# Optimization experiments

Measured on AMD Instinct MI355X. Metric: run time of the kernel, lower is better.

Reference implementation:

```python
import jax, jax.numpy as jnp
import numpy as np

B, C_IN, C_INTER, H, W_DIM = 8, 512, 256, 64, 64


def setup_inputs() -> dict:
    key = jax.random.key(0)
    k1, k2, k3, k4 = jax.random.split(key, 4)
    x = jax.random.normal(k1, (B, C_IN, H, W_DIM), dtype=jnp.float32)
    pem_feats = jax.random.normal(k2, (B, C_INTER, H * W_DIM), dtype=jnp.float32)
    # 1x1 conv weight stored as [out, in] (kernel spatial dims are 1x1)
    W = jax.random.normal(k3, (C_INTER, C_IN), dtype=jnp.float32) * (1.0 / np.sqrt(C_IN))
    bias = jax.random.normal(k4, (C_INTER,), dtype=jnp.float32) * 0.01
    return {"x": x, "pem_feats": pem_feats, "W": W, "bias": bias}


def reference(x, pem_feats, W, bias):
    b, c, h, w = x.shape
    # 1x1 conv == channel-mixing GEMM: [b, inter, h, w]
    proj = jnp.einsum('bchw,oc->bohw', x, W) + bias[None, :, None, None]
    proj = proj.reshape(b, -1, h * w)                      # [b, inter, hw]
    # weights[b,i,j] = <proj[:, i], pem[:, j]>  -> [b, hw, hw], softmax over j
    scores = jnp.einsum('bci,bcj->bij', proj, pem_feats)
    weights = jax.nn.softmax(scores, axis=-1)
    # out[b,k,i] = sum_j weights[b,j,i] * pem[b,k,j]
    eam = jnp.einsum('bji,bkj->bki', weights, pem_feats)   # [b, inter, hw]
    return eam.reshape(b, -1, h, w)
```

## Files before the change

kernel.cpp:

```cpp
#include <hip/hip_runtime.h>
#include <math.h>

#define BATCH 8
#define CIN 512
#define CO 256
#define HW 4096
#define KT 32
#define NSEG 4
#define SEGC 32

typedef unsigned short ushort_t;
typedef unsigned int uint_t;
typedef _Float16 v8h __attribute__((ext_vector_type(8)));
typedef _Float16 v4h __attribute__((ext_vector_type(4)));
typedef float v4f __attribute__((ext_vector_type(4)));
typedef ushort_t u16x8 __attribute__((ext_vector_type(8)));

__device__ __forceinline__ ushort_t f2h(float f) {
  return __builtin_bit_cast(ushort_t, (_Float16)f);
}
__device__ __forceinline__ v4f mfma16h(v8h a, v8h b, v4f c) {
  return __builtin_amdgcn_mfma_f32_16x16x32_f16(a, b, c, 0, 0, 0);
}
__device__ __forceinline__ v8h lds_frag_h512(const unsigned char* base, int row, int cb) {
  uint4 v = *(const uint4*)(base + row * 512 + (((cb) ^ (row & 7)) << 4));
  return __builtin_bit_cast(v8h, v);
}
__device__ __forceinline__ v8h lds_frag_h128(const unsigned char* base, int row, int cb) {
  uint4 v = *(const uint4*)(base + row * 128 + (((cb) ^ (row & 7)) << 4));
  return __builtin_bit_cast(v8h, v);
}
__device__ __forceinline__ void gll16(const void* g, void* l) {
  __builtin_amdgcn_global_load_lds(
      (const __attribute__((address_space(1))) unsigned int*)g,
      (__attribute__((address_space(3))) unsigned int*)l, 16, 0, 0);
}

__global__ __launch_bounds__(256) void k_w(
    const float* __restrict__ W, ushort_t* __restrict__ w_h) {
  int idx = blockIdx.x * 256 + threadIdx.x;
  size_t off = (size_t)idx * 8;
  float4 v0 = *(const float4*)&W[off];
  float4 v1 = *(const float4*)&W[off + 4];
  float f[8] = {v0.x, v0.y, v0.z, v0.w, v1.x, v1.y, v1.z, v1.w};
  u16x8 h;
#pragma unroll
  for (int j = 0; j < 8; ++j) h[j] = f2h(f[j]);
  *(u16x8*)&w_h[off] = h;
}

__global__ __launch_bounds__(256) void k_tr_x(
    const float* __restrict__ x, ushort_t* __restrict__ xt_h) {
  __shared__ float T[64][65];
  const int i0 = blockIdx.x * 64;
  const int c0 = blockIdx.y * 64;
  const int b  = blockIdx.z;
  const int t  = threadIdx.x;
  const int cl = t >> 4;
  const int i4 = (t & 15) * 4;
#pragma unroll
  for (int r = 0; r < 4; ++r) {
    int c = c0 + r * 16 + cl;
    size_t off = ((size_t)b * CIN + c) * HW + i0 + i4;
    float4 v = *(const float4*)&x[off];
    T[r * 16 + cl][i4 + 0] = v.x;
    T[r * 16 + cl][i4 + 1] = v.y;
    T[r * 16 + cl][i4 + 2] = v.z;
    T[r * 16 + cl][i4 + 3] = v.w;
  }
  __syncthreads();
  {
    int il = t >> 2;
    int cs = (t & 3) * 16;
    u16x8 h0, h1;
#pragma unroll
    for (int j = 0; j < 8; ++j) h0[j] = f2h(T[cs + j][il]);
#pragma unroll
    for (int j = 0; j < 8; ++j) h1[j] = f2h(T[cs + 8 + j][il]);
    size_t ro = ((size_t)b * HW + i0 + il) * CIN + c0 + cs;
    *(u16x8*)&xt_h[ro]     = h0;
    *(u16x8*)&xt_h[ro + 8] = h1;
  }
}

__global__ __launch_bounds__(256, 2) void k_proj_mfma(
    const ushort_t* __restrict__ xt_h, const ushort_t* __restrict__ w_h,
    const float* __restrict__ bias, ushort_t* __restrict__ proj_h) {
  __shared__ __align__(16) unsigned char L[2][128 * 128];
  const int bid = blockIdx.x;
  const int b = bid & 7;
  const int rest = bid >> 3;
  const int xt = rest & 31;
  const int oh = rest >> 5;
  const int x0 = xt * 128;
  const int t = threadIdx.x;
  const int lane = t & 63, wave = t >> 6;

  v4f acc[2][8];
#pragma unroll
  for (int xf = 0; xf < 2; ++xf)
#pragma unroll
    for (int of = 0; of < 8; ++of) acc[xf][of] = (v4f){0.f, 0.f, 0.f, 0.f};

  float bias_of[8];
#pragma unroll
  for (int of = 0; of < 8; ++of)
    bias_of[of] = bias[oh * 128 + of * 16 + (lane & 15)];

  for (int ch = 0; ch < 8; ++ch) {
    const int c0 = ch * 64;
#pragma unroll
    for (int i = 0; i < 4; ++i) {
      int G = i * 256 + t;
      int r = G >> 3, sl = G & 7;
      int cg = (sl ^ (r & 7)) << 3;
      size_t xsrc = ((size_t)b * HW + x0 + r) * CIN + c0 + cg;
      size_t wsrc = ((size_t)(oh * 128 + r)) * CIN + c0 + cg;
      unsigned lb = (unsigned)((i * 256 + wave * 64) << 4);
      gll16(&xt_h[xsrc], &L[0][lb]);
      gll16(&w_h[wsrc],  &L[1][lb]);
    }
    __syncthreads();
#pragma unroll
    for (int st = 0; st < 2; ++st) {
      int cb = st * 4 + (lane >> 4);
      v8h ah0 = lds_frag_h128(L[0], wave * 32 + (lane & 15), cb);
      v8h ah1 = lds_frag_h128(L[0], wave * 32 + 16 + (lane & 15), cb);
#pragma unroll
      for (int of = 0; of < 8; ++of) {
        v8h bh = lds_frag_h128(L[1], of * 16 + (lane & 15), cb);
        acc[0][of] = mfma16h(ah0, bh, acc[0][of]);
        acc[1][of] = mfma16h(ah1, bh, acc[1][of]);
      }
    }
    __syncthreads();
  }

  ushort_t* Th = (ushort_t*)&L[0][0];
#pragma unroll
  for (int xf = 0; xf < 2; ++xf)
#pragma unroll
    for (int of = 0; of < 8; ++of)
#pragma unroll
      for (int r = 0; r < 4; ++r) {
        int x_loc = wave * 32 + xf * 16 + (lane >> 4) * 4 + r;
        int o_loc = of * 16 + (lane & 15);
        Th[x_loc * 128 + o_loc] = f2h(acc[xf][of][r] + bias_of[of]);
      }
  __syncthreads();
  {
    int row = t >> 1, half = t & 1;
    size_t off = ((size_t)b * HW + x0 + row) * CO + oh * 128 + half * 64;
#pragma unroll
    for (int j = 0; j < 8; ++j)
      *(uint4*)&proj_h[off + j * 8] =
          *(const uint4*)&Th[row * 128 + half * 64 + j * 8];
  }
}

__global__ __launch_bounds__(256) void k_tr_pem(
    const float* __restrict__ pem,
    ushort_t* __restrict__ pem_t_h, ushort_t* __restrict__ pem_h) {
  __shared__ float T[64][65];
  const int y0 = blockIdx.x * 64;
  const int c0 = blockIdx.y * 64;
  const int b  = blockIdx.z;
  const int t  = threadIdx.x;
  const int cl = t >> 4;
  const int y4 = (t & 15) * 4;
#pragma unroll
  for (int r = 0; r < 4; ++r) {
    int c = c0 + r * 16 + cl;
    size_t off = ((size_t)b * CO + c) * HW + y0 + y4;
    float4 v = *(const float4*)&pem[off];
    ushort4 h;
    h.x = f2h(v.x); h.y = f2h(v.y); h.z = f2h(v.z); h.w = f2h(v.w);
    *(ushort4*)&pem_h[off] = h;
    T[r * 16 + cl][y4 + 0] = v.x;
    T[r * 16 + cl][y4 + 1] = v.y;
    T[r * 16 + cl][y4 + 2] = v.z;
    T[r * 16 + cl][y4 + 3] = v.w;
  }
  __syncthreads();
  {
    int yl = t >> 2;
    int cs = (t & 3) * 16;
    u16x8 h0, h1;
#pragma unroll
    for (int j = 0; j < 8; ++j) h0[j] = f2h(T[cs + j][yl]);
#pragma unroll
    for (int j = 0; j < 8; ++j) h1[j] = f2h(T[cs + 8 + j][yl]);
    size_t ro = ((size_t)b * HW + y0 + yl) * CO + c0 + cs;
    *(u16x8*)&pem_t_h[ro]     = h0;
    *(u16x8*)&pem_t_h[ro + 8] = h1;
  }
}

__global__ __launch_bounds__(512, 2) void k_stats_f16(
    const ushort_t* __restrict__ proj_h, const ushort_t* __restrict__ pem_t_h,
    float* __restrict__ m_seg, float* __restrict__ d_seg) {
  __shared__ __align__(16) unsigned char pbuf[2][32 * 512];
  const int id = blockIdx.x;
  const int b = id & 7;
  const int rest = id >> 3;
  const int xt = rest & 7;
  const int seg = rest >> 3;
  const int x0 = xt * 512;
  const int t = threadIdx.x;
  const int lane = t & 63, wave = t >> 6;
  const int xw = x0 + wave * 64;

  v8h Ah[4][8];
#pragma unroll
  for (int xf = 0; xf < 4; ++xf) {
    const size_t ro =
        ((size_t)b * HW + xw + xf * 16 + (lane & 15)) * CO + (lane >> 4) * 8;
#pragma unroll
    for (int st = 0; st < 8; ++st)
      Ah[xf][st] = __builtin_bit_cast(v8h, *(const uint4*)&proj_h[ro + st * 32]);
  }

  float m[4][4], d[4][4];
#pragma unroll
  for (int xf = 0; xf < 4; ++xf)
#pragma unroll
    for (int r = 0; r < 4; ++r) { m[xf][r] = -3.0e38f; d[xf][r] = 0.f; }

  auto stage = [&](int bufi, int tt) {
    const int yy0 = tt * 32;
#pragma unroll
    for (int i = 0; i < 2; ++i) {
      int G = i * 512 + t;
      int r = G >> 5, sl = G & 31;
      size_t so = ((size_t)b * HW + yy0 + r) * CO + ((sl ^ (r & 7)) << 3);
      unsigned lb = (unsigned)((i * 512 + wave * 64) << 4);
      gll16(&pem_t_h[so], &pbuf[bufi][lb]);
    }
  };

  const int tt0 = seg * SEGC;
  stage(0, tt0);
  __syncthreads();

  for (int tc = 0; tc < SEGC; ++tc) {
    if (tc + 1 < SEGC) stage((tc + 1) & 1, tt0 + tc + 1);

    const unsigned char* bp = pbuf[tc & 1];
    v4f acc[4][2];
#pragma unroll
    for (int xf = 0; xf < 4; ++xf)
#pragma unroll
      for (int yc = 0; yc < 2; ++yc) acc[xf][yc] = (v4f){0.f, 0.f, 0.f, 0.f};

#pragma unroll
    for (int st = 0; st < 8; ++st) {
#pragma unroll
      for (int yc = 0; yc < 2; ++yc) {
        v8h bh = lds_frag_h512(bp, yc * 16 + (lane & 15), st * 4 + (lane >> 4));
        acc[0][yc] = mfma16h(Ah[0][st], bh, acc[0][yc]);
        acc[1][yc] = mfma16h(Ah[1][st], bh, acc[1][yc]);
        acc[2][yc] = mfma16h(Ah[2][st], bh, acc[2][yc]);
        acc[3][yc] = mfma16h(Ah[3][st], bh, acc[3][yc]);
      }
    }

#pragma unroll
    for (int xf = 0; xf < 4; ++xf) {
      float mx8 = fmaxf(fmaxf(fmaxf(acc[xf][0][0], acc[xf][0][1]),
                              fmaxf(acc[xf][0][2], acc[xf][0][3])),
                        fmaxf(fmaxf(acc[xf][1][0], acc[xf][1][1]),
                              fmaxf(acc[xf][1][2], acc[xf][1][3])));
      float minm = fminf(fminf(m[xf][0], m[xf][1]), fminf(m[xf][2], m[xf][3]));
      if (__any(mx8 > minm + 8.0f)) {
#pragma unroll
        for (int r = 0; r < 4; ++r) {
          float rm = fmaxf(acc[xf][0][r], acc[xf][1][r]);
          rm = fmaxf(rm, __shfl_xor(rm, 1));
          rm = fmaxf(rm, __shfl_xor(rm, 2));
          rm = fmaxf(rm, __shfl_xor(rm, 4));
          rm = fmaxf(rm, __shfl_xor(rm, 8));
          float mn = fmaxf(m[xf][r], rm);
          d[xf][r] *= __expf(m[xf][r] - mn);
          m[xf][r] = mn;
        }
      }
#pragma unroll
      for (int r = 0; r < 4; ++r)
        d[xf][r] += __expf(acc[xf][0][r] - m[xf][r]) +
                    __expf(acc[xf][1][r] - m[xf][r]);
    }
    __syncthreads();
  }

#pragma unroll
  for (int xf = 0; xf < 4; ++xf) {
    float dv[4];
#pragma unroll
    for (int r = 0; r < 4; ++r) {
      float v = d[xf][r];
      v += __shfl_xor(v, 1);
      v += __shfl_xor(v, 2);
      v += __shfl_xor(v, 4);
      v += __shfl_xor(v, 8);
      dv[r] = v;
    }
    if ((lane & 15) == 0) {
      size_t o = ((size_t)(b * NSEG + seg)) * HW + xw + xf * 16 + (lane >> 4) * 4;
      *(float4*)&m_seg[o] = make_float4(m[xf][0], m[xf][1], m[xf][2], m[xf][3]);
      *(float4*)&d_seg[o] = make_float4(dv[0], dv[1], dv[2], dv[3]);
    }
  }
}

__global__ __launch_bounds__(256) void k_red2(
    const float* __restrict__ m_seg, const float* __restrict__ d_seg,
    float* __restrict__ Cx) {
  int idx = blockIdx.x * 256 + threadIdx.x;
  int b = idx >> 12;
  int xx = idx & 4095;
  float ms[NSEG], ds[NSEG];
  float mm = -3.0e38f;
#pragma unroll
  for (int s = 0; s < NSEG; ++s) {
    ms[s] = m_seg[((size_t)(b * NSEG + s)) * HW + xx];
    ds[s] = d_seg[((size_t)(b * NSEG + s)) * HW + xx];
    mm = fmaxf(mm, ms[s]);
  }
  float dd = 0.f;
#pragma unroll
  for (int s = 0; s < NSEG; ++s) dd += ds[s] * __expf(ms[s] - mm);
  Cx[(size_t)b * HW + xx] = mm + __logf(dd);
}

__global__ __launch_bounds__(512, 2) void k_fused(
    const ushort_t* __restrict__ proj_h, const ushort_t* __restrict__ pem_t_h,
    const ushort_t* __restrict__ pem_h, const float* __restrict__ Cx,
    float* __restrict__ out) {
  __shared__ __align__(16) unsigned char Lp[2][64 * 512];
  __shared__ __align__(16) unsigned char Lk[2][256 * 128];
  __shared__ __align__(16) unsigned char Le[128 * 128];
  const int id = blockIdx.x;
  const int b = id & 7;
  const int yt = id >> 3;
  const int y0 = yt * 128;
  const int t = threadIdx.x;
  const int lane = t & 63, wave = t >> 6;

  v8h Bres[8];
  {
    const size_t ro =
        ((size_t)b * HW + y0 + wave * 16 + (lane & 15)) * CO + (lane >> 4) * 8;
#pragma unroll
    for (int st = 0; st < 8; ++st)
      Bres[st] = __builtin_bit_cast(v8h, *(const uint4*)&pem_t_h[ro + st * 32]);
  }

  v4f pv[2][8];
#pragma unroll
  for (int kf = 0; kf < 2; ++kf)
#pragma unroll
    for (int yf = 0; yf < 8; ++yf) pv[kf][yf] = (v4f){0.f, 0.f, 0.f, 0.f};

  auto stage = [&](int bufi, int xt) {
    const int x0 = xt * 64;
#pragma unroll
    for (int i = 0; i < 4; ++i) {
      int G = i * 512 + t;
      int r = G >> 5, sl = G & 31;
      size_t so = ((size_t)b * HW + x0 + r) * CO + ((sl ^ (r & 7)) << 3);
      gll16(&proj_h[so], &Lp[bufi][(unsigned)((i * 512 + wave * 64) << 4)]);
    }
#pragma unroll
    for (int i = 0; i < 4; ++i) {
      int G = i * 512 + t;
      int r = G >> 3, sl = G & 7;
      size_t so = ((size_t)b * CO + r) * HW + x0 + ((sl ^ (r & 7)) << 3);
      gll16(&pem_h[so], &Lk[bufi][(unsigned)((i * 512 + wave * 64) << 4)]);
    }
  };

  stage(0, 0);

  for (int xt = 0; xt < 64; ++xt) {
    const int cur = xt & 1;
    const int x0 = xt * 64;
    __syncthreads();

    v4f s[4];
#pragma unroll
    for (int xf = 0; xf < 4; ++xf) s[xf] = (v4f){0.f, 0.f, 0.f, 0.f};
#pragma unroll
    for (int st = 0; st < 8; ++st) {
      int cb = st * 4 + (lane >> 4);
      v8h bh = Bres[st];
      s[0] = mfma16h(lds_frag_h512(Lp[cur], 0  + (lane & 15), cb), bh, s[0]);
      s[1] = mfma16h(lds_frag_h512(Lp[cur], 16 + (lane & 15), cb), bh, s[1]);
      s[2] = mfma16h(lds_frag_h512(Lp[cur], 32 + (lane & 15), cb), bh, s[2]);
      s[3] = mfma16h(lds_frag_h512(Lp[cur], 48 + (lane & 15), cb), bh, s[3]);
    }
    {
      int yl = wave * 16 + (lane & 15);
      int half = (lane >> 4) & 1;
      int gbase = (lane >> 4) >> 1;
#pragma unroll
      for (int xf = 0; xf < 4; ++xf) {
        float4 c4 = *(const float4*)&Cx[(size_t)b * HW + x0 + xf * 16 +
                                        (lane >> 4) * 4];
        float cc[4] = {c4.x, c4.y, c4.z, c4.w};
        v4h p;
#pragma unroll
        for (int r = 0; r < 4; ++r) p[r] = (_Float16)__expf(s[xf][r] - cc[r]);
        int gx = xf * 2 + gbase;
        *(uint2*)(Le + yl * 128 + ((gx ^ (yl & 7)) << 4) + half * 8) =
            __builtin_bit_cast(uint2, p);
      }
    }
    __syncthreads();

    if (xt + 1 < 64) stage(cur ^ 1, xt + 1);

    const int kb = wave * 32;
#pragma unroll
    for (int ks = 0; ks < 2; ++ks) {
      int cb = ks * 4 + (lane >> 4);
      v8h e[8];
#pragma unroll
      for (int yf = 0; yf < 8; ++yf)
        e[yf] = lds_frag_h128(Le, yf * 16 + (lane & 15), cb);
#pragma unroll
      for (int kf = 0; kf < 2; ++kf) {
        v8h af = lds_frag_h128(Lk[cur], kb + kf * 16 + (lane & 15), cb);
#pragma unroll
        for (int yf = 0; yf < 8; ++yf)
          pv[kf][yf] = mfma16h(af, e[yf], pv[kf][yf]);
      }
    }
  }

#pragma unroll
  for (int kf = 0; kf < 2; ++kf)
#pragma unroll
    for (int yf = 0; yf < 8; ++yf)
#pragma unroll
      for (int r = 0; r < 4; ++r) {
        int k = wave * 32 + kf * 16 + (lane >> 4) * 4 + r;
        int y = y0 + yf * 16 + (lane & 15);
        out[((size_t)b * CO + k) * HW + y] = pv[kf][yf][r];
      }
}

__global__ __launch_bounds__(256) void k_proj(
    const float* __restrict__ x, const float* __restrict__ W,
    const float* __restrict__ bias, float* __restrict__ proj) {
  __shared__ float As[KT][68];
  __shared__ float Bs[KT][68];
  const int i0 = blockIdx.x * 64;
  const int o0 = blockIdx.y * 64;
  const int b  = blockIdx.z;
  const int t  = threadIdx.x;
  const int tx = t & 15, ty = t >> 4;
  const float* xb = x + (size_t)b * CIN * HW;
  float acc[4][4] = {};
  for (int c0 = 0; c0 < CIN; c0 += KT) {
#pragma unroll
    for (int l = 0; l < 8; ++l) {
      int idx = t + l * 256;
      int o = idx >> 5;
      int c = idx & 31;
      As[c][o] = W[(size_t)(o0 + o) * CIN + c0 + c];
    }
#pragma unroll
    for (int l = 0; l < 2; ++l) {
      int idx4 = t + l * 256;
      int c = idx4 >> 4;
      int i4 = idx4 & 15;
      *(float4*)&Bs[c][i4 * 4] =
          *(const float4*)&xb[(size_t)(c0 + c) * HW + i0 + i4 * 4];
    }
    __syncthreads();
#pragma unroll
    for (int c = 0; c < KT; ++c) {
      float4 a  = *(const float4*)&As[c][tx * 4];
      float4 bv = *(const float4*)&Bs[c][ty * 4];
      float av[4] = {a.x, a.y, a.z, a.w};
      float bb[4] = {bv.x, bv.y, bv.z, bv.w};
#pragma unroll
      for (int u = 0; u < 4; ++u)
#pragma unroll
        for (int v = 0; v < 4; ++v) acc[u][v] += av[u] * bb[v];
    }
    __syncthreads();
  }
  float* pbout = proj + (size_t)b * CO * HW;
#pragma unroll
  for (int u = 0; u < 4; ++u) {
    int o = o0 + tx * 4 + u;
    float bsv = bias[o];
    float4 r;
    r.x = acc[u][0] + bsv; r.y = acc[u][1] + bsv;
    r.z = acc[u][2] + bsv; r.w = acc[u][3] + bsv;
    *(float4*)&pbout[(size_t)o * HW + i0 + ty * 4] = r;
  }
}

__global__ __launch_bounds__(256) void k_stats(
    const float* __restrict__ proj, const float* __restrict__ pem,
    float* __restrict__ Mx, float* __restrict__ Dinv) {
  __shared__ float As[KT][68];
  __shared__ float Bs[KT][68];
  __shared__ float MsS[64][17];
  __shared__ float DsS[64][17];
  const int x0 = blockIdx.x * 64;
  const int b  = blockIdx.y;
  const int t  = threadIdx.x;
  const int tx = t & 15, ty = t >> 4;
  const float* pj = proj + (size_t)b * CO * HW;
  const float* pe = pem + (size_t)b * CO * HW;
  float m[4], d[4];
#pragma unroll
  for (int u = 0; u < 4; ++u) { m[u] = -3.0e38f; d[u] = 0.f; }
  for (int y0 = 0; y0 < HW; y0 += 64) {
    float s[4][4] = {};
    for (int c0 = 0; c0 < CO; c0 += KT) {
#pragma unroll
      for (int l = 0; l < 2; ++l) {
        int idx4 = t + l * 256;
        int c = idx4 >> 4, w4 = idx4 & 15;
        *(float4*)&As[c][w4 * 4] =
            *(const float4*)&pj[(size_t)(c0 + c) * HW + x0 + w4 * 4];
        *(float4*)&Bs[c][w4 * 4] =
            *(const float4*)&pe[(size_t)(c0 + c) * HW + y0 + w4 * 4];
      }
      __syncthreads();
#pragma unroll
      for (int c = 0; c < KT; ++c) {
        float4 a  = *(const float4*)&As[c][tx * 4];
        float4 bv = *(const float4*)&Bs[c][ty * 4];
        float av[4] = {a.x, a.y, a.z, a.w};
        float bb[4] = {bv.x, bv.y, bv.z, bv.w};
#pragma unroll
        for (int u = 0; u < 4; ++u)
#pragma unroll
          for (int v = 0; v < 4; ++v) s[u][v] += av[u] * bb[v];
      }
      __syncthreads();
    }
#pragma unroll
    for (int u = 0; u < 4; ++u) {
      float mv = fmaxf(fmaxf(s[u][0], s[u][1]), fmaxf(s[u][2], s[u][3]));
      if (mv > m[u]) { d[u] *= __expf(m[u] - mv); m[u] = mv; }
      d[u] += __expf(s[u][0] - m[u]) + __expf(s[u][1] - m[u]) +
              __expf(s[u][2] - m[u]) + __expf(s[u][3] - m[u]);
    }
  }
#pragma unroll
  for (int u = 0; u < 4; ++u) { MsS[tx * 4 + u][ty] = m[u]; DsS[tx * 4 + u][ty] = d[u]; }
  __syncthreads();
  if (t < 64) {
    float mm = -3.0e38f;
#pragma unroll
    for (int i = 0; i < 16; ++i) mm = fmaxf(mm, MsS[t][i]);
    float dd = 0.f;
#pragma unroll
    for (int i = 0; i < 16; ++i) dd += DsS[t][i] * __expf(MsS[t][i] - mm);
    Mx[(size_t)b * HW + x0 + t]   = mm;
    Dinv[(size_t)b * HW + x0 + t] = 1.0f / dd;
  }
}

__global__ __launch_bounds__(256) void k_out(
    const float* __restrict__ proj, const float* __restrict__ pem,
    const float* __restrict__ Mx, const float* __restrict__ Dinv,
    float* __restrict__ out) {
  __shared__ float As[KT][68];
  __shared__ float Bs[KT][68];
  __shared__ float E[64][68];
  const int y0 = blockIdx.x * 64;
  const int b  = blockIdx.y;
  const int t  = threadIdx.x;
  const int tx = t & 15, ty = t >> 4;
  const int kg = t >> 3, yg = t & 7;
  const float* pj = proj + (size_t)b * CO * HW;
  const float* pe = pem + (size_t)b * CO * HW;
  const float* Mb = Mx + (size_t)b * HW;
  const float* Db = Dinv + (size_t)b * HW;
  float acc[8][8] = {};
  for (int x0 = 0; x0 < HW; x0 += 64) {
    float s[4][4] = {};
    for (int c0 = 0; c0 < CO; c0 += KT) {
#pragma unroll
      for (int l = 0; l < 2; ++l) {
        int idx4 = t + l * 256;
        int c = idx4 >> 4, w4 = idx4 & 15;
        *(float4*)&As[c][w4 * 4] =
            *(const float4*)&pj[(size_t)(c0 + c) * HW + x0 + w4 * 4];
        *(float4*)&Bs[c][w4 * 4] =
            *(const float4*)&pe[(size_t)(c0 + c) * HW + y0 + w4 * 4];
      }
      __syncthreads();
#pragma unroll
      for (int c = 0; c < KT; ++c) {
        float4 a  = *(const float4*)&As[c][tx * 4];
        float4 bv = *(const float4*)&Bs[c][ty * 4];
        float av[4] = {a.x, a.y, a.z, a.w};
        float bb[4] = {bv.x, bv.y, bv.z, bv.w};
#pragma unroll
        for (int u = 0; u < 4; ++u)
#pragma unroll
          for (int v = 0; v < 4; ++v) s[u][v] += av[u] * bb[v];
      }
      __syncthreads();
    }
#pragma unroll
    for (int u = 0; u < 4; ++u) {
      int xr = x0 + tx * 4 + u;
      float mm = Mb[xr];
      float di = Db[xr];
      E[tx * 4 + u][ty * 4 + 0] = __expf(s[u][0] - mm) * di;
      E[tx * 4 + u][ty * 4 + 1] = __expf(s[u][1] - mm) * di;
      E[tx * 4 + u][ty * 4 + 2] = __expf(s[u][2] - mm) * di;
      E[tx * 4 + u][ty * 4 + 3] = __expf(s[u][3] - mm) * di;
    }
    __syncthreads();
    for (int xi = 0; xi < 64; xi += 4) {
      float4 p[8];
#pragma unroll
      for (int u = 0; u < 8; ++u)
        p[u] = *(const float4*)&pe[(size_t)(kg * 8 + u) * HW + x0 + xi];
#pragma unroll
      for (int j = 0; j < 4; ++j) {
        float4 e0 = *(const float4*)&E[xi + j][yg * 8];
        float4 e1 = *(const float4*)&E[xi + j][yg * 8 + 4];
        float evv[8] = {e0.x, e0.y, e0.z, e0.w, e1.x, e1.y, e1.z, e1.w};
#pragma unroll
        for (int u = 0; u < 8; ++u) {
          float a = (j == 0) ? p[u].x : (j == 1) ? p[u].y : (j == 2) ? p[u].z : p[u].w;
#pragma unroll
          for (int v = 0; v < 8; ++v) acc[u][v] += a * evv[v];
        }
      }
    }
    __syncthreads();
  }
#pragma unroll
  for (int u = 0; u < 8; ++u) {
    int k = kg * 8 + u;
    float4 r0, r1;
    r0.x = acc[u][0]; r0.y = acc[u][1]; r0.z = acc[u][2]; r0.w = acc[u][3];
    r1.x = acc[u][4]; r1.y = acc[u][5]; r1.z = acc[u][6]; r1.w = acc[u][7];
    float* ob = out + ((size_t)b * CO + k) * HW + y0 + yg * 8;
    *(float4*)&ob[0] = r0;
    *(float4*)&ob[4] = r1;
  }
}

extern "C" void kernel_launch(void* const* d_in, const int* in_sizes, int n_in,
                              void* d_out, int out_size, void* d_ws, size_t ws_size,
                              hipStream_t stream) {
  const float* x    = (const float*)d_in[0];
  const float* pem  = (const float*)d_in[1];
  const float* W    = (const float*)d_in[2];
  const float* bias = (const float*)d_in[3];
  float* out = (float*)d_out;

  const size_t NS   = (size_t)BATCH * HW * CO;
  const size_t NS2  = (size_t)BATCH * HW * CIN;
  const size_t HWB  = (size_t)BATCH * HW;
  const size_t SEGN = (size_t)BATCH * NSEG * HW;
  const size_t WN   = (size_t)CO * CIN;

  unsigned char* basep = (unsigned char*)d_ws;
  ushort_t* proj_h   = (ushort_t*)basep;
  ushort_t* pem_t_h  = proj_h + NS;
  ushort_t* pem_h    = pem_t_h + NS;
  float*    Cxp      = (float*)(pem_h + NS);
  float*    m_seg    = Cxp + HWB;
  float*    d_seg    = m_seg + SEGN;
  ushort_t* xt_h     = (ushort_t*)(d_seg + SEGN);
  ushort_t* w_h      = xt_h + NS2;

  const size_t need = 3 * NS * 2 + HWB * 4 + 2 * SEGN * 4 + NS2 * 2 + WN * 2;

  if (ws_size < need) {
    float* proj = (float*)d_ws;
    float* Mx2  = proj + NS;
    float* Di2  = Mx2 + HWB;
    const size_t need_f = (NS + 2 * HWB) * sizeof(float);
    if (ws_size < need_f) return;
    k_proj <<<dim3(HW / 64, CO / 64, BATCH), 256, 0, stream>>>(x, W, bias, proj);
    k_stats<<<dim3(HW / 64, BATCH),          256, 0, stream>>>(proj, pem, Mx2, Di2);
    k_out  <<<dim3(HW / 64, BATCH),          256, 0, stream>>>(proj, pem, Mx2, Di2, out);
    return;
  }

  k_w<<<64, 256, 0, stream>>>(W, w_h);
  k_tr_x<<<dim3(HW / 64, CIN / 64, BATCH), 256, 0, stream>>>(x, xt_h);
  k_proj_mfma<<<512, 256, 0, stream>>>(xt_h, w_h, bias, proj_h);
  k_tr_pem<<<dim3(HW / 64, CO / 64, BATCH), 256, 0, stream>>>(pem, pem_t_h, pem_h);

  k_stats_f16<<<256, 512, 0, stream>>>(proj_h, pem_t_h, m_seg, d_seg);
  k_red2<<<128, 256, 0, stream>>>(m_seg, d_seg, Cxp);
  k_fused<<<256, 512, 0, stream>>>(proj_h, pem_t_h, pem_h, Cxp, out);
}
```

Before: 327.2 us.

## Switch fused attention kernel to 32x32x16 MFMA tiles with new wave partitioning

Replaces the 16x16x32 f16 MFMA tiles in both GEMMs of the fused kernel with 32x32x16 MFMA. The waves are repartitioned into 2x4 (score) and 4x2 (output) grids, which cuts LDS fragment loads per FLOP and raises operand reuse. It also wraps the MFMA loops in s_setprio to favour the matrix issue. In exchange, more registers are held per wave (Bres doubled, 64-float accumulators), which risks spills or lower occupancy under the 512x2 launch bounds.

```diff
diff --git a/kernel.cpp b/kernel.cpp
--- a/kernel.cpp
+++ b/kernel.cpp
@@ -14,6 +14,7 @@
 typedef _Float16 v8h __attribute__((ext_vector_type(8)));
 typedef _Float16 v4h __attribute__((ext_vector_type(4)));
 typedef float v4f __attribute__((ext_vector_type(4)));
+typedef float v16f __attribute__((ext_vector_type(16)));
 typedef ushort_t u16x8 __attribute__((ext_vector_type(8)));
 
 __device__ __forceinline__ ushort_t f2h(float f) {
@@ -21,6 +22,9 @@
 }
 __device__ __forceinline__ v4f mfma16h(v8h a, v8h b, v4f c) {
   return __builtin_amdgcn_mfma_f32_16x16x32_f16(a, b, c, 0, 0, 0);
+}
+__device__ __forceinline__ v16f mfma32h(v8h a, v8h b, v16f c) {
+  return __builtin_amdgcn_mfma_f32_32x32x16_f16(a, b, c, 0, 0, 0);
 }
 __device__ __forceinline__ v8h lds_frag_h512(const unsigned char* base, int row, int cb) {
   uint4 v = *(const uint4*)(base + row * 512 + (((cb) ^ (row & 7)) << 4));
@@ -345,21 +349,26 @@
   const int y0 = yt * 128;
   const int t = threadIdx.x;
   const int lane = t & 63, wave = t >> 6;
-
-  v8h Bres[8];
+  const int l31 = lane & 31, lh = lane >> 5;
+  const int wx = wave & 1, wy = wave >> 1;
+  const int kq = wave & 3, yq = wave >> 2;
+
+  v8h Bres[16];
   {
     const size_t ro =
-        ((size_t)b * HW + y0 + wave * 16 + (lane & 15)) * CO + (lane >> 4) * 8;
-#pragma unroll
-    for (int st = 0; st < 8; ++st)
-      Bres[st] = __builtin_bit_cast(v8h, *(const uint4*)&pem_t_h[ro + st * 32]);
-  }
-
-  v4f pv[2][8];
-#pragma unroll
-  for (int kf = 0; kf < 2; ++kf)
-#pragma unroll
-    for (int yf = 0; yf < 8; ++yf) pv[kf][yf] = (v4f){0.f, 0.f, 0.f, 0.f};
+        ((size_t)b * HW + y0 + wy * 32 + l31) * CO + lh * 8;
+#pragma unroll
+    for (int st = 0; st < 16; ++st)
+      Bres[st] = __builtin_bit_cast(v8h, *(const uint4*)&pem_t_h[ro + st * 16]);
+  }
+
+  v16f pv[2][2];
+#pragma unroll
+  for (int kt = 0; kt < 2; ++kt)
+#pragma unroll
+    for (int yy = 0; yy < 2; ++yy)
+#pragma unroll
+      for (int r = 0; r < 16; ++r) pv[kt][yy][r] = 0.f;
 
   auto stage = [&](int bufi, int xt) {
     const int x0 = xt * 64;
@@ -386,32 +395,30 @@
     const int x0 = xt * 64;
     __syncthreads();
 
-    v4f s[4];
-#pragma unroll
-    for (int xf = 0; xf < 4; ++xf) s[xf] = (v4f){0.f, 0.f, 0.f, 0.f};
-#pragma unroll
-    for (int st = 0; st < 8; ++st) {
-      int cb = st * 4 + (lane >> 4);
-      v8h bh = Bres[st];
-      s[0] = mfma16h(lds_frag_h512(Lp[cur], 0  + (lane & 15), cb), bh, s[0]);
-      s[1] = mfma16h(lds_frag_h512(Lp[cur], 16 + (lane & 15), cb), bh, s[1]);
-      s[2] = mfma16h(lds_frag_h512(Lp[cur], 32 + (lane & 15), cb), bh, s[2]);
-      s[3] = mfma16h(lds_frag_h512(Lp[cur], 48 + (lane & 15), cb), bh, s[3]);
-    }
+    v16f s;
+#pragma unroll
+    for (int r = 0; r < 16; ++r) s[r] = 0.f;
+    __builtin_amdgcn_s_setprio(1);
+#pragma unroll
+    for (int st = 0; st < 16; ++st) {
+      v8h a = lds_frag_h512(Lp[cur], wx * 32 + l31, st * 2 + lh);
+      s = mfma32h(a, Bres[st], s);
+    }
+    __builtin_amdgcn_s_setprio(0);
+
     {
-      int yl = wave * 16 + (lane & 15);
-      int half = (lane >> 4) & 1;
-      int gbase = (lane >> 4) >> 1;
-#pragma unroll
-      for (int xf = 0; xf < 4; ++xf) {
-        float4 c4 = *(const float4*)&Cx[(size_t)b * HW + x0 + xf * 16 +
-                                        (lane >> 4) * 4];
+      int erow = wy * 32 + l31;
+#pragma unroll
+      for (int q = 0; q < 4; ++q) {
+        int xg = x0 + wx * 32 + 8 * q + 4 * lh;
+        float4 c4 = *(const float4*)&Cx[(size_t)b * HW + xg];
         float cc[4] = {c4.x, c4.y, c4.z, c4.w};
         v4h p;
 #pragma unroll
-        for (int r = 0; r < 4; ++r) p[r] = (_Float16)__expf(s[xf][r] - cc[r]);
-        int gx = xf * 2 + gbase;
-        *(uint2*)(Le + yl * 128 + ((gx ^ (yl & 7)) << 4) + half * 8) =
+        for (int r = 0; r < 4; ++r)
+          p[r] = (_Float16)__expf(s[4 * q + r] - cc[r]);
+        int gx = wx * 4 + q;
+        *(uint2*)(Le + erow * 128 + ((gx ^ (erow & 7)) << 4) + lh * 8) =
             __builtin_bit_cast(uint2, p);
       }
     }
@@ -419,33 +426,31 @@
 
     if (xt + 1 < 64) stage(cur ^ 1, xt + 1);
 
-    const int kb = wave * 32;
-#pragma unroll
-    for (int ks = 0; ks < 2; ++ks) {
-      int cb = ks * 4 + (lane >> 4);
-      v8h e[8];
-#pragma unroll
-      for (int yf = 0; yf < 8; ++yf)
-        e[yf] = lds_frag_h128(Le, yf * 16 + (lane & 15), cb);
-#pragma unroll
-      for (int kf = 0; kf < 2; ++kf) {
-        v8h af = lds_frag_h128(Lk[cur], kb + kf * 16 + (lane & 15), cb);
-#pragma unroll
-        for (int yf = 0; yf < 8; ++yf)
-          pv[kf][yf] = mfma16h(af, e[yf], pv[kf][yf]);
-      }
-    }
-  }
-
-#pragma unroll
-  for (int kf = 0; kf < 2; ++kf)
-#pragma unroll
-    for (int yf = 0; yf < 8; ++yf)
-#pragma unroll
-      for (int r = 0; r < 4; ++r) {
-        int k = wave * 32 + kf * 16 + (lane >> 4) * 4 + r;
-        int y = y0 + yf * 16 + (lane & 15);
-        out[((size_t)b * CO + k) * HW + y] = pv[kf][yf][r];
+    __builtin_amdgcn_s_setprio(1);
+#pragma unroll
+    for (int st = 0; st < 4; ++st) {
+      int cb = st * 2 + lh;
+      v8h e0 = lds_frag_h128(Le, yq * 64 + l31, cb);
+      v8h e1 = lds_frag_h128(Le, yq * 64 + 32 + l31, cb);
+      v8h a0 = lds_frag_h128(Lk[cur], kq * 64 + l31, cb);
+      v8h a1 = lds_frag_h128(Lk[cur], kq * 64 + 32 + l31, cb);
+      pv[0][0] = mfma32h(a0, e0, pv[0][0]);
+      pv[0][1] = mfma32h(a0, e1, pv[0][1]);
+      pv[1][0] = mfma32h(a1, e0, pv[1][0]);
+      pv[1][1] = mfma32h(a1, e1, pv[1][1]);
+    }
+    __builtin_amdgcn_s_setprio(0);
+  }
+
+#pragma unroll
+  for (int kt = 0; kt < 2; ++kt)
+#pragma unroll
+    for (int yy = 0; yy < 2; ++yy)
+#pragma unroll
+      for (int r = 0; r < 16; ++r) {
+        int k = kq * 64 + kt * 32 + (r & 3) + 8 * (r >> 2) + 4 * lh;
+        int y = y0 + yq * 64 + yy * 32 + l31;
+        out[((size_t)b * CO + k) * HW + y] = pv[kt][yy][r];
       }
 }
 
```

New measurement: 321.9 us. No clear change (-1.6%).
